# Kernel optimization log

Measured on AMD Instinct MI355X. Metric: run time of the kernel, lower is better.

Reference implementation:

```python
import jax, jax.numpy as jnp
import numpy as np

D_MODEL = 1024
N_HEADS = 16
HEAD_DIM = D_MODEL // N_HEADS


def setup_inputs() -> dict:
    key = jax.random.key(0)
    ks = jax.random.split(key, 9)
    B, T = 2, 2048
    s = 1.0 / np.sqrt(D_MODEL)
    x = jax.random.normal(ks[0], (B, T, D_MODEL), dtype=jnp.float32)
    Wq = jax.random.uniform(ks[1], (D_MODEL, D_MODEL), jnp.float32, -s, s)
    bq = jax.random.uniform(ks[2], (D_MODEL,), jnp.float32, -s, s)
    Wk = jax.random.uniform(ks[3], (D_MODEL, D_MODEL), jnp.float32, -s, s)
    bk = jax.random.uniform(ks[4], (D_MODEL,), jnp.float32, -s, s)
    Wv = jax.random.uniform(ks[5], (D_MODEL, D_MODEL), jnp.float32, -s, s)
    bv = jax.random.uniform(ks[6], (D_MODEL,), jnp.float32, -s, s)
    Wp = jax.random.uniform(ks[7], (D_MODEL, D_MODEL), jnp.float32, -s, s)
    bp = jax.random.uniform(ks[8], (D_MODEL,), jnp.float32, -s, s)
    return {"x": x, "Wq": Wq, "bq": bq, "Wk": Wk, "bk": bk,
            "Wv": Wv, "bv": bv, "Wp": Wp, "bp": bp}


def reference(x, Wq, bq, Wk, bk, Wv, bv, Wp, bp):
    B, T, C = x.shape
    H, Dh = N_HEADS, HEAD_DIM
    # torch Linear: x @ W.T + b
    q = (x @ Wq.T + bq).reshape(B, T, H, Dh).transpose(0, 2, 1, 3)  # [B,H,T,Dh]
    k = (x @ Wk.T + bk).reshape(B, T, H, Dh).transpose(0, 2, 1, 3)
    v = (x @ Wv.T + bv).reshape(B, T, H, Dh).transpose(0, 2, 1, 3)
    scale = 1.0 / np.sqrt(Dh).astype(np.float32)
    att = jnp.einsum('bhqd,bhkd->bhqk', q, k) * scale  # [B,H,T,T]
    causal = jnp.tril(jnp.ones((T, T), dtype=bool))
    att = jnp.where(causal[None, None], att, -jnp.inf)
    att = jax.nn.softmax(att, axis=-1)
    y = jnp.einsum('bhqk,bhkd->bhqd', att, v)  # [B,H,T,Dh]
    y = y.transpose(0, 2, 1, 3).reshape(B, T, C)
    return y @ Wp.T + bp
```

## Files before the change

### kernel.cpp

```cpp
#include <hip/hip_runtime.h>
#include <hip/hip_bf16.h>
#include <math.h>

#define D_MODEL 1024
#define N_HEADS 16
#define HEAD_DIM 64
#define SEQ_T 2048
#define BATCH 2

typedef __attribute__((ext_vector_type(8))) short short8;
typedef __attribute__((ext_vector_type(4))) float f32x4;

__device__ __forceinline__ unsigned short f2bf(float f) {
    union { float f; unsigned int u; } v; v.f = f;
    return (unsigned short)((v.u + 0x7FFFu + ((v.u >> 16) & 1u)) >> 16);
}

__device__ __forceinline__ void glds16(const unsigned short* g, unsigned short* l) {
    __builtin_amdgcn_global_load_lds(
        (const __attribute__((address_space(1))) unsigned int*)g,
        (__attribute__((address_space(3))) unsigned int*)l, 16, 0, 0);
}

__global__ void cvt_all(const float4* __restrict__ x,
                        const float4* __restrict__ Wq, const float4* __restrict__ Wk,
                        const float4* __restrict__ Wv, const float4* __restrict__ Wp,
                        ushort4* __restrict__ xb, ushort4* __restrict__ wb,
                        ushort4* __restrict__ wpb) {
    int i = blockIdx.x * 256 + threadIdx.x;
    float4 v; ushort4* dst;
    if (i < 1048576) { v = x[i]; dst = xb + i; }
    else {
        int j = i - 1048576;
        int wsel = j >> 18;
        int o = j & 262143;
        const float4* s = wsel == 0 ? Wq : wsel == 1 ? Wk : wsel == 2 ? Wv : Wp;
        v = s[o];
        dst = (wsel == 3) ? (wpb + o) : (wb + (size_t)wsel * 262144 + o);
    }
    ushort4 u;
    u.x = f2bf(v.x); u.y = f2bf(v.y); u.z = f2bf(v.z); u.w = f2bf(v.w);
    *dst = u;
}

template<int MODE, int MTILE>
__global__ __launch_bounds__(256) void gemm2(
    const unsigned short* __restrict__ A,
    const unsigned short* __restrict__ W,
    const float* __restrict__ b0, const float* __restrict__ b1, const float* __restrict__ b2,
    void* __restrict__ o0, void* __restrict__ o1, void* __restrict__ o2)
{
    constexpr int K = 1024;
    constexpr int MT = MTILE / 32;
    constexpr int CAW = MTILE / 64;
    __shared__ unsigned short As[MTILE * 32];
    __shared__ unsigned short Bs[128 * 32];
    const int m0 = blockIdx.y * MTILE;
    const int n0 = blockIdx.x * 128;
    const int tid = threadIdx.x;
    const int w = tid >> 6, lane = tid & 63;
    const int col = lane & 15, quad = lane >> 4;
    const int wm = (w & 1) * (MTILE / 2), wn = (w >> 1) * 64;
    const int lr = lane >> 2, lc = (lane & 3) * 8;

    const f32x4 zero = {0.f, 0.f, 0.f, 0.f};
    f32x4 acc[MT][4];
#pragma unroll
    for (int i = 0; i < MT; i++)
#pragma unroll
        for (int j = 0; j < 4; j++) acc[i][j] = zero;

    for (int k0 = 0; k0 < K; k0 += 32) {
        __syncthreads();
#pragma unroll
        for (int c = 0; c < CAW; c++) {
            const int q = w * CAW + c;
            glds16(&A[(size_t)(m0 + q * 16 + lr) * K + k0 + lc], &As[q * 512]);
        }
#pragma unroll
        for (int c = 0; c < 2; c++) {
            const int q = w * 2 + c;
            glds16(&W[(size_t)(n0 + q * 16 + lr) * K + k0 + lc], &Bs[q * 512]);
        }
        __syncthreads();
        short8 af[MT], bf[4];
#pragma unroll
        for (int mt = 0; mt < MT; mt++)
            af[mt] = *(const short8*)&As[(wm + mt * 16 + col) * 32 + quad * 8];
#pragma unroll
        for (int nt = 0; nt < 4; nt++)
            bf[nt] = *(const short8*)&Bs[(wn + nt * 16 + col) * 32 + quad * 8];
#pragma unroll
        for (int mt = 0; mt < MT; mt++)
#pragma unroll
            for (int nt = 0; nt < 4; nt++)
                acc[mt][nt] = __builtin_amdgcn_mfma_f32_16x16x32_bf16(af[mt], bf[nt], acc[mt][nt], 0, 0, 0);
    }

#pragma unroll
    for (int mt = 0; mt < MT; mt++) {
#pragma unroll
        for (int nt = 0; nt < 4; nt++) {
            const int n = n0 + wn + nt * 16 + col;
            float bias;
            if constexpr (MODE == 2) bias = b0[n];
            else {
                const int sel = n >> 10, nq = n & 1023;
                bias = (sel == 0 ? b0 : sel == 1 ? b1 : b2)[nq];
            }
#pragma unroll
            for (int r = 0; r < 4; r++) {
                const int m = m0 + wm + mt * 16 + quad * 4 + r;
                const float v = acc[mt][nt][r] + bias;
                if constexpr (MODE == 2) {
                    ((float*)o0)[(size_t)m * 1024 + n] = v;
                } else {
                    const int sel = n >> 10, nq = n & 1023;
                    const int h = nq >> 6, dh = nq & 63, b = m >> 11, t = m & 2047;
                    if (sel < 2) {
                        unsigned short* dst = sel ? (unsigned short*)o1 : (unsigned short*)o0;
                        int tt = t;
                        if (sel == 1) {
                            const int tb = t & 31;
                            tt = (t & ~31) + ((tb & 4) << 2) + ((tb >> 3) << 2) + (tb & 3);
                        }
                        dst[(((size_t)(b * N_HEADS + h)) * SEQ_T + tt) * HEAD_DIM + dh] = f2bf(v);
                    } else {
                        ((unsigned short*)o2)[((size_t)(b * N_HEADS + h) * HEAD_DIM + dh) * SEQ_T + t] = f2bf(v);
                    }
                }
            }
        }
    }
}

__global__ __launch_bounds__(256) void flash8(
    const unsigned short* __restrict__ Q,
    const unsigned short* __restrict__ Kp,
    const unsigned short* __restrict__ Vt,
    unsigned short* __restrict__ Y)
{
    __shared__ unsigned short Ks[2][64 * 64];
    __shared__ unsigned short Vs[2][64 * 64];

    const int tid = threadIdx.x;
    const int w = tid >> 6, lane = tid & 63;
    const int col = lane & 15, quad = lane >> 4;
    const int i = blockIdx.x;
    const int bh = (i & 7) * 4 + ((i >> 3) & 3);
    const int qtp = i >> 5;
    const int b = bh >> 4, h = bh & 15;

    const unsigned short* qbase = Q + (size_t)bh * SEQ_T * HEAD_DIM;
    const unsigned short* kbase = Kp + (size_t)bh * SEQ_T * HEAD_DIM;
    const unsigned short* vbase = Vt + (size_t)bh * HEAD_DIM * SEQ_T;

    const int srow = lane >> 3;
    const int schunk = (lane & 7) ^ srow;
    const int cswz = col & 7;

    const float SC2 = 0.18033688011f;
    const f32x4 zero = {0.f, 0.f, 0.f, 0.f};

    for (int ti = 0; ti < 2; ti++) {
        const int qt = ti ? (31 - qtp) : qtp;
        const int qrow = qt * 64 + w * 16;
        const short8 qf0 = *(const short8*)&qbase[(size_t)(qrow + col) * HEAD_DIM + quad * 8];
        const short8 qf1 = *(const short8*)&qbase[(size_t)(qrow + col) * HEAD_DIM + quad * 8 + 32];

        f32x4 acc[4];
#pragma unroll
        for (int nt = 0; nt < 4; nt++) acc[nt] = zero;
        float l = 0.f;

        const int nk = qt + 1;

        __syncthreads();
#pragma unroll
        for (int rq = 0; rq < 2; rq++) {
            const int rr = rq * 32 + 8 * w;
            glds16(&kbase[(size_t)(rr + srow) * HEAD_DIM + schunk * 8], &Ks[0][rr * 64]);
            glds16(&vbase[(size_t)(rr + srow) * SEQ_T + schunk * 8], &Vs[0][rr * 64]);
        }

        int cur = 0;
        for (int kt = 0; kt < nk; kt++) {
            const int kb = kt * 64;
            __syncthreads();

            if (kt + 1 < nk) {
                const int kb2 = kb + 64;
#pragma unroll
                for (int rq = 0; rq < 2; rq++) {
                    const int rr = rq * 32 + 8 * w;
                    glds16(&kbase[(size_t)(kb2 + rr + srow) * HEAD_DIM + schunk * 8], &Ks[cur ^ 1][rr * 64]);
                    glds16(&vbase[(size_t)(rr + srow) * SEQ_T + kb2 + schunk * 8], &Vs[cur ^ 1][rr * 64]);
                }
            }

            const unsigned short* ks = Ks[cur];
            const unsigned short* vs = Vs[cur];

            short8 vB[2][4];
#pragma unroll
            for (int g = 0; g < 2; g++)
#pragma unroll
                for (int nt = 0; nt < 4; nt++)
                    vB[g][nt] = *(const short8*)&vs[(nt * 16 + col) * 64 + (((g * 4 + quad) ^ cswz) * 8)];

            f32x4 St[4];
            __builtin_amdgcn_s_setprio(1);
#pragma unroll
            for (int kc = 0; kc < 4; kc++) {
                const short8 kf0 = *(const short8*)&ks[(kc * 16 + col) * 64 + ((quad ^ cswz) * 8)];
                const short8 kf1 = *(const short8*)&ks[(kc * 16 + col) * 64 + (((quad + 4) ^ cswz) * 8)];
                f32x4 z = zero;
                z = __builtin_amdgcn_mfma_f32_16x16x32_bf16(kf0, qf0, z, 0, 0, 0);
                z = __builtin_amdgcn_mfma_f32_16x16x32_bf16(kf1, qf1, z, 0, 0, 0);
                St[kc] = z;
            }
            __builtin_amdgcn_s_setprio(0);

            short8 pA[2];
            if (kt == nk - 1) {
#pragma unroll
                for (int g = 0; g < 2; g++) {
                    union { short8 s; __hip_bfloat162 h[4]; } pu;
#pragma unroll
                    for (int t16 = 0; t16 < 2; t16++) {
                        const int kc = 2 * g + t16;
                        const int kbase_c = kb + (kc >> 1) * 32 + quad * 8 + (kc & 1) * 4;
                        float p[4];
#pragma unroll
                        for (int r = 0; r < 4; r++) {
                            p[r] = __builtin_amdgcn_exp2f(St[kc][r] * SC2);
                            if (kbase_c + r > qrow + col) p[r] = 0.f;
                            l += p[r];
                        }
                        pu.h[t16 * 2]     = __float22bfloat162_rn(make_float2(p[0], p[1]));
                        pu.h[t16 * 2 + 1] = __float22bfloat162_rn(make_float2(p[2], p[3]));
                    }
                    pA[g] = pu.s;
                }
            } else {
#pragma unroll
                for (int g = 0; g < 2; g++) {
                    union { short8 s; __hip_bfloat162 h[4]; } pu;
#pragma unroll
                    for (int t16 = 0; t16 < 2; t16++) {
                        const int kc = 2 * g + t16;
                        float p[4];
#pragma unroll
                        for (int r = 0; r < 4; r++) {
                            p[r] = __builtin_amdgcn_exp2f(St[kc][r] * SC2);
                            l += p[r];
                        }
                        pu.h[t16 * 2]     = __float22bfloat162_rn(make_float2(p[0], p[1]));
                        pu.h[t16 * 2 + 1] = __float22bfloat162_rn(make_float2(p[2], p[3]));
                    }
                    pA[g] = pu.s;
                }
            }

            __builtin_amdgcn_s_setprio(1);
#pragma unroll
            for (int g = 0; g < 2; g++)
#pragma unroll
                for (int nt = 0; nt < 4; nt++)
                    acc[nt] = __builtin_amdgcn_mfma_f32_16x16x32_bf16(pA[g], vB[g][nt], acc[nt], 0, 0, 0);
            __builtin_amdgcn_s_setprio(0);

            cur ^= 1;
        }

        l += __shfl_xor(l, 16);
        l += __shfl_xor(l, 32);
        const float linv = 1.0f / l;
        float lr[4];
#pragma unroll
        for (int r = 0; r < 4; r++) lr[r] = __shfl(linv, quad * 4 + r);
#pragma unroll
        for (int nt = 0; nt < 4; nt++)
#pragma unroll
            for (int r = 0; r < 4; r++) {
                const int qg = qrow + quad * 4 + r;
                Y[((size_t)(b * SEQ_T + qg)) * D_MODEL + h * HEAD_DIM + nt * 16 + col] = f2bf(acc[nt][r] * lr[r]);
            }
    }
}

extern "C" void kernel_launch(void* const* d_in, const int* in_sizes, int n_in,
                              void* d_out, int out_size, void* d_ws, size_t ws_size,
                              hipStream_t stream) {
    const float* x  = (const float*)d_in[0];
    const float* Wq = (const float*)d_in[1];
    const float* bq = (const float*)d_in[2];
    const float* Wk = (const float*)d_in[3];
    const float* bk = (const float*)d_in[4];
    const float* Wv = (const float*)d_in[5];
    const float* bv = (const float*)d_in[6];
    const float* Wp = (const float*)d_in[7];
    const float* bp = (const float*)d_in[8];
    float* out = (float*)d_out;

    char* ws = (char*)d_ws;
    const size_t XSZ = (size_t)4096 * 1024 * 2;
    unsigned short* xb  = (unsigned short*)ws;  ws += XSZ;
    unsigned short* wb  = (unsigned short*)ws;  ws += (size_t)3072 * 1024 * 2;
    unsigned short* wpb = (unsigned short*)ws;  ws += (size_t)1024 * 1024 * 2;
    unsigned short* qb  = (unsigned short*)ws;  ws += XSZ;
    unsigned short* kb  = (unsigned short*)ws;  ws += XSZ;
    unsigned short* vtb = (unsigned short*)ws;  ws += XSZ;
    unsigned short* yb  = (unsigned short*)ws;  ws += XSZ;

    cvt_all<<<8192, 256, 0, stream>>>((const float4*)x, (const float4*)Wq, (const float4*)Wk,
                                      (const float4*)Wv, (const float4*)Wp,
                                      (ushort4*)xb, (ushort4*)wb, (ushort4*)wpb);

    gemm2<3, 128><<<dim3(24, 32), 256, 0, stream>>>(xb, wb, bq, bk, bv, qb, kb, vtb);

    flash8<<<512, 256, 0, stream>>>(qb, kb, vtb, yb);

    gemm2<2, 64><<<dim3(8, 64), 256, 0, stream>>>(yb, wpb, bp, nullptr, nullptr, out, nullptr, nullptr);
}
```

Baseline: 184.6 us.

## Enlarge flash attention query tile to 128 rows per block for K/V reuse

Each block now handles 128 query rows, with each wave computing two 16-row sub-tiles, so every K/V tile loaded into shared memory is reused across twice as many queries. The grid is halved to 256 blocks, and causal pairing is redone over 16 super-tiles. Waves whose rows lie entirely above a key tile skip its compute. In exchange, register pressure rises, parallelism drops (256 blocks on a 256-CU device), and wave load becomes imbalanced within the diagonal tiles.

```diff
diff --git a/kernel.cpp b/kernel.cpp
--- a/kernel.cpp
+++ b/kernel.cpp
@@ -134,7 +134,7 @@
     }
 }
 
-__global__ __launch_bounds__(256) void flash8(
+__global__ __launch_bounds__(256) void flash9(
     const unsigned short* __restrict__ Q,
     const unsigned short* __restrict__ Kp,
     const unsigned short* __restrict__ Vt,
@@ -148,7 +148,7 @@
     const int col = lane & 15, quad = lane >> 4;
     const int i = blockIdx.x;
     const int bh = (i & 7) * 4 + ((i >> 3) & 3);
-    const int qtp = i >> 5;
+    const int sp = i >> 5;
     const int b = bh >> 4, h = bh & 15;
 
     const unsigned short* qbase = Q + (size_t)bh * SEQ_T * HEAD_DIM;
@@ -163,17 +163,23 @@
     const f32x4 zero = {0.f, 0.f, 0.f, 0.f};
 
     for (int ti = 0; ti < 2; ti++) {
-        const int qt = ti ? (31 - qtp) : qtp;
-        const int qrow = qt * 64 + w * 16;
-        const short8 qf0 = *(const short8*)&qbase[(size_t)(qrow + col) * HEAD_DIM + quad * 8];
-        const short8 qf1 = *(const short8*)&qbase[(size_t)(qrow + col) * HEAD_DIM + quad * 8 + 32];
-
-        f32x4 acc[4];
-#pragma unroll
-        for (int nt = 0; nt < 4; nt++) acc[nt] = zero;
-        float l = 0.f;
-
-        const int nk = qt + 1;
+        const int s = ti ? (15 - sp) : sp;
+        const int qrow = s * 128 + w * 32;
+        short8 qf[2][2];
+#pragma unroll
+        for (int m = 0; m < 2; m++) {
+            qf[m][0] = *(const short8*)&qbase[(size_t)(qrow + m * 16 + col) * HEAD_DIM + quad * 8];
+            qf[m][1] = *(const short8*)&qbase[(size_t)(qrow + m * 16 + col) * HEAD_DIM + quad * 8 + 32];
+        }
+
+        f32x4 acc[2][4];
+#pragma unroll
+        for (int m = 0; m < 2; m++)
+#pragma unroll
+            for (int nt = 0; nt < 4; nt++) acc[m][nt] = zero;
+        float l[2] = {0.f, 0.f};
+
+        const int nk = 2 * s + 2;
 
         __syncthreads();
 #pragma unroll
@@ -198,94 +204,109 @@
                 }
             }
 
-            const unsigned short* ks = Ks[cur];
-            const unsigned short* vs = Vs[cur];
-
-            short8 vB[2][4];
-#pragma unroll
-            for (int g = 0; g < 2; g++)
-#pragma unroll
-                for (int nt = 0; nt < 4; nt++)
-                    vB[g][nt] = *(const short8*)&vs[(nt * 16 + col) * 64 + (((g * 4 + quad) ^ cswz) * 8)];
-
-            f32x4 St[4];
-            __builtin_amdgcn_s_setprio(1);
-#pragma unroll
-            for (int kc = 0; kc < 4; kc++) {
-                const short8 kf0 = *(const short8*)&ks[(kc * 16 + col) * 64 + ((quad ^ cswz) * 8)];
-                const short8 kf1 = *(const short8*)&ks[(kc * 16 + col) * 64 + (((quad + 4) ^ cswz) * 8)];
-                f32x4 z = zero;
-                z = __builtin_amdgcn_mfma_f32_16x16x32_bf16(kf0, qf0, z, 0, 0, 0);
-                z = __builtin_amdgcn_mfma_f32_16x16x32_bf16(kf1, qf1, z, 0, 0, 0);
-                St[kc] = z;
+            if (kb <= qrow + 31) {
+                const unsigned short* ks = Ks[cur];
+                const unsigned short* vs = Vs[cur];
+
+                short8 vB[2][4];
+#pragma unroll
+                for (int g = 0; g < 2; g++)
+#pragma unroll
+                    for (int nt = 0; nt < 4; nt++)
+                        vB[g][nt] = *(const short8*)&vs[(nt * 16 + col) * 64 + (((g * 4 + quad) ^ cswz) * 8)];
+
+                f32x4 St[2][4];
+                __builtin_amdgcn_s_setprio(1);
+#pragma unroll
+                for (int kc = 0; kc < 4; kc++) {
+                    const short8 kf0 = *(const short8*)&ks[(kc * 16 + col) * 64 + ((quad ^ cswz) * 8)];
+                    const short8 kf1 = *(const short8*)&ks[(kc * 16 + col) * 64 + (((quad + 4) ^ cswz) * 8)];
+#pragma unroll
+                    for (int m = 0; m < 2; m++) {
+                        f32x4 z = zero;
+                        z = __builtin_amdgcn_mfma_f32_16x16x32_bf16(kf0, qf[m][0], z, 0, 0, 0);
+                        z = __builtin_amdgcn_mfma_f32_16x16x32_bf16(kf1, qf[m][1], z, 0, 0, 0);
+                        St[m][kc] = z;
+                    }
+                }
+                __builtin_amdgcn_s_setprio(0);
+
+                const bool needMask = (kb + 63 > qrow);
+#pragma unroll
+                for (int m = 0; m < 2; m++) {
+                    const int qq = qrow + m * 16 + col;
+                    short8 pA[2];
+                    if (needMask) {
+#pragma unroll
+                        for (int g = 0; g < 2; g++) {
+                            union { short8 s; __hip_bfloat162 h[4]; } pu;
+#pragma unroll
+                            for (int t16 = 0; t16 < 2; t16++) {
+                                const int kc = 2 * g + t16;
+                                const int kbase_c = kb + (kc >> 1) * 32 + quad * 8 + (kc & 1) * 4;
+                                float p[4];
+#pragma unroll
+                                for (int r = 0; r < 4; r++) {
+                                    p[r] = __builtin_amdgcn_exp2f(St[m][kc][r] * SC2);
+                                    if (kbase_c + r > qq) p[r] = 0.f;
+                                    l[m] += p[r];
+                                }
+                                pu.h[t16 * 2]     = __float22bfloat162_rn(make_float2(p[0], p[1]));
+                                pu.h[t16 * 2 + 1] = __float22bfloat162_rn(make_float2(p[2], p[3]));
+                            }
+                            pA[g] = pu.s;
+                        }
+                    } else {
+#pragma unroll
+                        for (int g = 0; g < 2; g++) {
+                            union { short8 s; __hip_bfloat162 h[4]; } pu;
+#pragma unroll
+                            for (int t16 = 0; t16 < 2; t16++) {
+                                const int kc = 2 * g + t16;
+                                float p[4];
+#pragma unroll
+                                for (int r = 0; r < 4; r++) {
+                                    p[r] = __builtin_amdgcn_exp2f(St[m][kc][r] * SC2);
+                                    l[m] += p[r];
+                                }
+                                pu.h[t16 * 2]     = __float22bfloat162_rn(make_float2(p[0], p[1]));
+                                pu.h[t16 * 2 + 1] = __float22bfloat162_rn(make_float2(p[2], p[3]));
+                            }
+                            pA[g] = pu.s;
+                        }
+                    }
+
+                    __builtin_amdgcn_s_setprio(1);
+#pragma unroll
+                    for (int g = 0; g < 2; g++)
+#pragma unroll
+                        for (int nt = 0; nt < 4; nt++)
+                            acc[m][nt] = __builtin_amdgcn_mfma_f32_16x16x32_bf16(pA[g], vB[g][nt], acc[m][nt], 0, 0, 0);
+                    __builtin_amdgcn_s_setprio(0);
+                }
             }
-            __builtin_amdgcn_s_setprio(0);
-
-            short8 pA[2];
-            if (kt == nk - 1) {
-#pragma unroll
-                for (int g = 0; g < 2; g++) {
-                    union { short8 s; __hip_bfloat162 h[4]; } pu;
-#pragma unroll
-                    for (int t16 = 0; t16 < 2; t16++) {
-                        const int kc = 2 * g + t16;
-                        const int kbase_c = kb + (kc >> 1) * 32 + quad * 8 + (kc & 1) * 4;
-                        float p[4];
-#pragma unroll
-                        for (int r = 0; r < 4; r++) {
-                            p[r] = __builtin_amdgcn_exp2f(St[kc][r] * SC2);
-                            if (kbase_c + r > qrow + col) p[r] = 0.f;
-                            l += p[r];
-                        }
-                        pu.h[t16 * 2]     = __float22bfloat162_rn(make_float2(p[0], p[1]));
-                        pu.h[t16 * 2 + 1] = __float22bfloat162_rn(make_float2(p[2], p[3]));
-                    }
-                    pA[g] = pu.s;
-                }
-            } else {
-#pragma unroll
-                for (int g = 0; g < 2; g++) {
-                    union { short8 s; __hip_bfloat162 h[4]; } pu;
-#pragma unroll
-                    for (int t16 = 0; t16 < 2; t16++) {
-                        const int kc = 2 * g + t16;
-                        float p[4];
-#pragma unroll
-                        for (int r = 0; r < 4; r++) {
-                            p[r] = __builtin_amdgcn_exp2f(St[kc][r] * SC2);
-                            l += p[r];
-                        }
-                        pu.h[t16 * 2]     = __float22bfloat162_rn(make_float2(p[0], p[1]));
-                        pu.h[t16 * 2 + 1] = __float22bfloat162_rn(make_float2(p[2], p[3]));
-                    }
-                    pA[g] = pu.s;
-                }
-            }
-
-            __builtin_amdgcn_s_setprio(1);
-#pragma unroll
-            for (int g = 0; g < 2; g++)
-#pragma unroll
-                for (int nt = 0; nt < 4; nt++)
-                    acc[nt] = __builtin_amdgcn_mfma_f32_16x16x32_bf16(pA[g], vB[g][nt], acc[nt], 0, 0, 0);
-            __builtin_amdgcn_s_setprio(0);
 
             cur ^= 1;
         }
 
-        l += __shfl_xor(l, 16);
-        l += __shfl_xor(l, 32);
-        const float linv = 1.0f / l;
-        float lr[4];
-#pragma unroll
-        for (int r = 0; r < 4; r++) lr[r] = __shfl(linv, quad * 4 + r);
-#pragma unroll
-        for (int nt = 0; nt < 4; nt++)
-#pragma unroll
-            for (int r = 0; r < 4; r++) {
-                const int qg = qrow + quad * 4 + r;
-                Y[((size_t)(b * SEQ_T + qg)) * D_MODEL + h * HEAD_DIM + nt * 16 + col] = f2bf(acc[nt][r] * lr[r]);
-            }
+#pragma unroll
+        for (int m = 0; m < 2; m++) {
+            float lm = l[m];
+            lm += __shfl_xor(lm, 16);
+            lm += __shfl_xor(lm, 32);
+            const float linv = 1.0f / lm;
+            float lr[4];
+#pragma unroll
+            for (int r = 0; r < 4; r++) lr[r] = __shfl(linv, quad * 4 + r);
+#pragma unroll
+            for (int nt = 0; nt < 4; nt++)
+#pragma unroll
+                for (int r = 0; r < 4; r++) {
+                    const int qg = qrow + m * 16 + quad * 4 + r;
+                    Y[((size_t)(b * SEQ_T + qg)) * D_MODEL + h * HEAD_DIM + nt * 16 + col] =
+                        f2bf(acc[m][nt][r] * lr[r]);
+                }
+        }
     }
 }
 
@@ -319,7 +340,7 @@
 
     gemm2<3, 128><<<dim3(24, 32), 256, 0, stream>>>(xb, wb, bq, bk, bv, qb, kb, vtb);
 
-    flash8<<<512, 256, 0, stream>>>(qb, kb, vtb, yb);
+    flash9<<<256, 256, 0, stream>>>(qb, kb, vtb, yb);
 
     gemm2<2, 64><<<dim3(8, 64), 256, 0, stream>>>(yb, wpb, bp, nullptr, nullptr, out, nullptr, nullptr);
 }
```

Measured after the change: 195.0 us. +5.6%, slower.

## Split paired causal q-tiles into separate blocks with longest-first ordering

Applied to the files above, without the earlier changes.

Each flash block used to process two query tiles (qtp and 31-qtp) in sequence so that per-block work stayed balanced. Now each block handles one query tile, the grid doubles to 1024 blocks, and tiles are ordered so the heaviest ones (largest causal key range) launch first. This raises parallelism and lets the hardware scheduler balance load dynamically. The trade-off is more blocks, each reloading its own K/V prologue, and less deterministic per-block balance.

```diff
diff --git a/kernel.cpp b/kernel.cpp
--- a/kernel.cpp
+++ b/kernel.cpp
@@ -134,7 +134,7 @@
     }
 }
 
-__global__ __launch_bounds__(256) void flash8(
+__global__ __launch_bounds__(256) void flash11(
     const unsigned short* __restrict__ Q,
     const unsigned short* __restrict__ Kp,
     const unsigned short* __restrict__ Vt,
@@ -146,9 +146,13 @@
     const int tid = threadIdx.x;
     const int w = tid >> 6, lane = tid & 63;
     const int col = lane & 15, quad = lane >> 4;
-    const int i = blockIdx.x;
-    const int bh = (i & 7) * 4 + ((i >> 3) & 3);
-    const int qtp = i >> 5;
+
+    const int j = blockIdx.x >> 5;
+    const int x = j & 7, rnd = j >> 3;
+    const int qt = (rnd == 0) ? (31 - x) : (rnd == 1) ? (16 + x)
+                 : (rnd == 2) ? (15 - x) : x;
+    const int g = blockIdx.x & 31;
+    const int bh = (g & 7) * 4 + (g >> 3);
     const int b = bh >> 4, h = bh & 15;
 
     const unsigned short* qbase = Q + (size_t)bh * SEQ_T * HEAD_DIM;
@@ -162,131 +166,127 @@
     const float SC2 = 0.18033688011f;
     const f32x4 zero = {0.f, 0.f, 0.f, 0.f};
 
-    for (int ti = 0; ti < 2; ti++) {
-        const int qt = ti ? (31 - qtp) : qtp;
-        const int qrow = qt * 64 + w * 16;
-        const short8 qf0 = *(const short8*)&qbase[(size_t)(qrow + col) * HEAD_DIM + quad * 8];
-        const short8 qf1 = *(const short8*)&qbase[(size_t)(qrow + col) * HEAD_DIM + quad * 8 + 32];
-
-        f32x4 acc[4];
-#pragma unroll
-        for (int nt = 0; nt < 4; nt++) acc[nt] = zero;
-        float l = 0.f;
-
-        const int nk = qt + 1;
-
+    const int qrow = qt * 64 + w * 16;
+    const short8 qf0 = *(const short8*)&qbase[(size_t)(qrow + col) * HEAD_DIM + quad * 8];
+    const short8 qf1 = *(const short8*)&qbase[(size_t)(qrow + col) * HEAD_DIM + quad * 8 + 32];
+
+    f32x4 acc[4];
+#pragma unroll
+    for (int nt = 0; nt < 4; nt++) acc[nt] = zero;
+    float l = 0.f;
+
+    const int nk = qt + 1;
+
+#pragma unroll
+    for (int rq = 0; rq < 2; rq++) {
+        const int rr = rq * 32 + 8 * w;
+        glds16(&kbase[(size_t)(rr + srow) * HEAD_DIM + schunk * 8], &Ks[0][rr * 64]);
+        glds16(&vbase[(size_t)(rr + srow) * SEQ_T + schunk * 8], &Vs[0][rr * 64]);
+    }
+
+    int cur = 0;
+    for (int kt = 0; kt < nk; kt++) {
+        const int kb = kt * 64;
         __syncthreads();
-#pragma unroll
-        for (int rq = 0; rq < 2; rq++) {
-            const int rr = rq * 32 + 8 * w;
-            glds16(&kbase[(size_t)(rr + srow) * HEAD_DIM + schunk * 8], &Ks[0][rr * 64]);
-            glds16(&vbase[(size_t)(rr + srow) * SEQ_T + schunk * 8], &Vs[0][rr * 64]);
-        }
-
-        int cur = 0;
-        for (int kt = 0; kt < nk; kt++) {
-            const int kb = kt * 64;
-            __syncthreads();
-
-            if (kt + 1 < nk) {
-                const int kb2 = kb + 64;
-#pragma unroll
-                for (int rq = 0; rq < 2; rq++) {
-                    const int rr = rq * 32 + 8 * w;
-                    glds16(&kbase[(size_t)(kb2 + rr + srow) * HEAD_DIM + schunk * 8], &Ks[cur ^ 1][rr * 64]);
-                    glds16(&vbase[(size_t)(rr + srow) * SEQ_T + kb2 + schunk * 8], &Vs[cur ^ 1][rr * 64]);
+
+        if (kt + 1 < nk) {
+            const int kb2 = kb + 64;
+#pragma unroll
+            for (int rq = 0; rq < 2; rq++) {
+                const int rr = rq * 32 + 8 * w;
+                glds16(&kbase[(size_t)(kb2 + rr + srow) * HEAD_DIM + schunk * 8], &Ks[cur ^ 1][rr * 64]);
+                glds16(&vbase[(size_t)(rr + srow) * SEQ_T + kb2 + schunk * 8], &Vs[cur ^ 1][rr * 64]);
+            }
+        }
+
+        const unsigned short* ks = Ks[cur];
+        const unsigned short* vs = Vs[cur];
+
+        short8 vB[2][4];
+#pragma unroll
+        for (int gg = 0; gg < 2; gg++)
+#pragma unroll
+            for (int nt = 0; nt < 4; nt++)
+                vB[gg][nt] = *(const short8*)&vs[(nt * 16 + col) * 64 + (((gg * 4 + quad) ^ cswz) * 8)];
+
+        f32x4 St[4];
+        __builtin_amdgcn_s_setprio(1);
+#pragma unroll
+        for (int kc = 0; kc < 4; kc++) {
+            const short8 kf0 = *(const short8*)&ks[(kc * 16 + col) * 64 + ((quad ^ cswz) * 8)];
+            const short8 kf1 = *(const short8*)&ks[(kc * 16 + col) * 64 + (((quad + 4) ^ cswz) * 8)];
+            f32x4 z = zero;
+            z = __builtin_amdgcn_mfma_f32_16x16x32_bf16(kf0, qf0, z, 0, 0, 0);
+            z = __builtin_amdgcn_mfma_f32_16x16x32_bf16(kf1, qf1, z, 0, 0, 0);
+            St[kc] = z;
+        }
+        __builtin_amdgcn_s_setprio(0);
+
+        short8 pA[2];
+        if (kt == nk - 1) {
+#pragma unroll
+            for (int gg = 0; gg < 2; gg++) {
+                union { short8 s; __hip_bfloat162 h[4]; } pu;
+#pragma unroll
+                for (int t16 = 0; t16 < 2; t16++) {
+                    const int kc = 2 * gg + t16;
+                    const int kbase_c = kb + (kc >> 1) * 32 + quad * 8 + (kc & 1) * 4;
+                    float p[4];
+#pragma unroll
+                    for (int r = 0; r < 4; r++) {
+                        p[r] = __builtin_amdgcn_exp2f(St[kc][r] * SC2);
+                        if (kbase_c + r > qrow + col) p[r] = 0.f;
+                        l += p[r];
+                    }
+                    pu.h[t16 * 2]     = __float22bfloat162_rn(make_float2(p[0], p[1]));
+                    pu.h[t16 * 2 + 1] = __float22bfloat162_rn(make_float2(p[2], p[3]));
                 }
-            }
-
-            const unsigned short* ks = Ks[cur];
-            const unsigned short* vs = Vs[cur];
-
-            short8 vB[2][4];
-#pragma unroll
-            for (int g = 0; g < 2; g++)
-#pragma unroll
-                for (int nt = 0; nt < 4; nt++)
-                    vB[g][nt] = *(const short8*)&vs[(nt * 16 + col) * 64 + (((g * 4 + quad) ^ cswz) * 8)];
-
-            f32x4 St[4];
-            __builtin_amdgcn_s_setprio(1);
-#pragma unroll
-            for (int kc = 0; kc < 4; kc++) {
-                const short8 kf0 = *(const short8*)&ks[(kc * 16 + col) * 64 + ((quad ^ cswz) * 8)];
-                const short8 kf1 = *(const short8*)&ks[(kc * 16 + col) * 64 + (((quad + 4) ^ cswz) * 8)];
-                f32x4 z = zero;
-                z = __builtin_amdgcn_mfma_f32_16x16x32_bf16(kf0, qf0, z, 0, 0, 0);
-                z = __builtin_amdgcn_mfma_f32_16x16x32_bf16(kf1, qf1, z, 0, 0, 0);
-                St[kc] = z;
-            }
-            __builtin_amdgcn_s_setprio(0);
-
-            short8 pA[2];
-            if (kt == nk - 1) {
-#pragma unroll
-                for (int g = 0; g < 2; g++) {
-                    union { short8 s; __hip_bfloat162 h[4]; } pu;
-#pragma unroll
-                    for (int t16 = 0; t16 < 2; t16++) {
-                        const int kc = 2 * g + t16;
-                        const int kbase_c = kb + (kc >> 1) * 32 + quad * 8 + (kc & 1) * 4;
-                        float p[4];
-#pragma unroll
-                        for (int r = 0; r < 4; r++) {
-                            p[r] = __builtin_amdgcn_exp2f(St[kc][r] * SC2);
-                            if (kbase_c + r > qrow + col) p[r] = 0.f;
-                            l += p[r];
-                        }
-                        pu.h[t16 * 2]     = __float22bfloat162_rn(make_float2(p[0], p[1]));
-                        pu.h[t16 * 2 + 1] = __float22bfloat162_rn(make_float2(p[2], p[3]));
+                pA[gg] = pu.s;
+            }
+        } else {
+#pragma unroll
+            for (int gg = 0; gg < 2; gg++) {
+                union { short8 s; __hip_bfloat162 h[4]; } pu;
+#pragma unroll
+                for (int t16 = 0; t16 < 2; t16++) {
+                    const int kc = 2 * gg + t16;
+                    float p[4];
+#pragma unroll
+                    for (int r = 0; r < 4; r++) {
+                        p[r] = __builtin_amdgcn_exp2f(St[kc][r] * SC2);
+                        l += p[r];
                     }
-                    pA[g] = pu.s;
+                    pu.h[t16 * 2]     = __float22bfloat162_rn(make_float2(p[0], p[1]));
+                    pu.h[t16 * 2 + 1] = __float22bfloat162_rn(make_float2(p[2], p[3]));
                 }
-            } else {
-#pragma unroll
-                for (int g = 0; g < 2; g++) {
-                    union { short8 s; __hip_bfloat162 h[4]; } pu;
-#pragma unroll
-                    for (int t16 = 0; t16 < 2; t16++) {
-                        const int kc = 2 * g + t16;
-                        float p[4];
-#pragma unroll
-                        for (int r = 0; r < 4; r++) {
-                            p[r] = __builtin_amdgcn_exp2f(St[kc][r] * SC2);
-                            l += p[r];
-                        }
-                        pu.h[t16 * 2]     = __float22bfloat162_rn(make_float2(p[0], p[1]));
-                        pu.h[t16 * 2 + 1] = __float22bfloat162_rn(make_float2(p[2], p[3]));
-                    }
-                    pA[g] = pu.s;
-                }
-            }
-
-            __builtin_amdgcn_s_setprio(1);
-#pragma unroll
-            for (int g = 0; g < 2; g++)
-#pragma unroll
-                for (int nt = 0; nt < 4; nt++)
-                    acc[nt] = __builtin_amdgcn_mfma_f32_16x16x32_bf16(pA[g], vB[g][nt], acc[nt], 0, 0, 0);
-            __builtin_amdgcn_s_setprio(0);
-
-            cur ^= 1;
-        }
-
-        l += __shfl_xor(l, 16);
-        l += __shfl_xor(l, 32);
-        const float linv = 1.0f / l;
-        float lr[4];
-#pragma unroll
-        for (int r = 0; r < 4; r++) lr[r] = __shfl(linv, quad * 4 + r);
-#pragma unroll
-        for (int nt = 0; nt < 4; nt++)
-#pragma unroll
-            for (int r = 0; r < 4; r++) {
-                const int qg = qrow + quad * 4 + r;
-                Y[((size_t)(b * SEQ_T + qg)) * D_MODEL + h * HEAD_DIM + nt * 16 + col] = f2bf(acc[nt][r] * lr[r]);
-            }
-    }
+                pA[gg] = pu.s;
+            }
+        }
+
+        __builtin_amdgcn_s_setprio(1);
+#pragma unroll
+        for (int gg = 0; gg < 2; gg++)
+#pragma unroll
+            for (int nt = 0; nt < 4; nt++)
+                acc[nt] = __builtin_amdgcn_mfma_f32_16x16x32_bf16(pA[gg], vB[gg][nt], acc[nt], 0, 0, 0);
+        __builtin_amdgcn_s_setprio(0);
+
+        cur ^= 1;
+    }
+
+    l += __shfl_xor(l, 16);
+    l += __shfl_xor(l, 32);
+    const float linv = 1.0f / l;
+    float lr[4];
+#pragma unroll
+    for (int r = 0; r < 4; r++) lr[r] = __shfl(linv, quad * 4 + r);
+#pragma unroll
+    for (int nt = 0; nt < 4; nt++)
+#pragma unroll
+        for (int r = 0; r < 4; r++) {
+            const int qg = qrow + quad * 4 + r;
+            Y[((size_t)(b * SEQ_T + qg)) * D_MODEL + h * HEAD_DIM + nt * 16 + col] = f2bf(acc[nt][r] * lr[r]);
+        }
 }
 
 extern "C" void kernel_launch(void* const* d_in, const int* in_sizes, int n_in,
@@ -319,7 +319,7 @@
 
     gemm2<3, 128><<<dim3(24, 32), 256, 0, stream>>>(xb, wb, bq, bk, bv, qb, kb, vtb);
 
-    flash8<<<512, 256, 0, stream>>>(qb, kb, vtb, yb);
+    flash11<<<1024, 256, 0, stream>>>(qb, kb, vtb, yb);
 
     gemm2<2, 64><<<dim3(8, 64), 256, 0, stream>>>(yb, wpb, bp, nullptr, nullptr, out, nullptr, nullptr);
 }
```

Result: no change. 184.0 us (-0.3%).
